# Kernel optimization log

Hardware: AMD Instinct MI355X
Metric: run time of the kernel (lower is better)

Reference implementation:

```python
import jax, jax.numpy as jnp
import numpy as np

N = 50000      # n_nodes == ninput
E = 800000     # edges
NHID = 96
N_INTER = 6
EPS = 1e-12


def _l2norm(x):
    # F.normalize(x, p=2, dim=1) with eps=1e-12
    n = jnp.linalg.norm(x, axis=1, keepdims=True)
    return x / jnp.maximum(n, EPS)


def _sage(x, src, dst, Wl, bl, Wr, n):
    # PyG SAGEConv (mean aggr): lin_l(mean_{j in N(i)} x_j) + lin_r(x_i)
    agg = jax.ops.segment_sum(x[src], dst, num_segments=n)          # [N, nhid]
    deg = jax.ops.segment_sum(jnp.ones((src.shape[0],), x.dtype), dst, num_segments=n)
    agg = agg / jnp.maximum(deg, 1.0)[:, None]
    return agg @ Wl + bl + x @ Wr


def _mlp(x, W1, b1, W2, b2, W3, b3):
    # GNN-Bet score MLP (eval mode, dropout p=0): nhid -> 2*nhid -> 2*nhid -> 1
    h = jax.nn.relu(x @ W1 + b1)
    h = jax.nn.relu(h @ W2 + b2)
    return h @ W3 + b3


def setup_inputs() -> dict:
    key = jax.random.key(0)
    ks = jax.random.split(key, 16)
    s = 0.05
    inp = {
        'edge_index1': jax.random.randint(ks[0], (2, E), 0, N, dtype=jnp.int32),
        'edge_vals1': jax.random.uniform(ks[1], (E,), dtype=jnp.float32),
        'edge_index2': jax.random.randint(ks[2], (2, E), 0, N, dtype=jnp.int32),
        # GNN_Layer_Init: weight [ninput=N, nhid], bias [nhid]
        'gc1_W': jax.random.normal(ks[3], (N, NHID), dtype=jnp.float32) * s,
        'gc1_b': jnp.zeros((NHID,), jnp.float32),
        # 7 SAGEConv layers (6 intermediate + gc_last), stacked
        'sage_Wl': jax.random.normal(ks[4], (7, NHID, NHID), dtype=jnp.float32) * s,
        'sage_bl': jnp.zeros((7, NHID), jnp.float32),
        'sage_Wr': jax.random.normal(ks[5], (7, NHID, NHID), dtype=jnp.float32) * s,
        # score MLP
        'mlp_W1': jax.random.normal(ks[6], (NHID, 2 * NHID), dtype=jnp.float32) * s,
        'mlp_b1': jnp.zeros((2 * NHID,), jnp.float32),
        'mlp_W2': jax.random.normal(ks[7], (2 * NHID, 2 * NHID), dtype=jnp.float32) * s,
        'mlp_b2': jnp.zeros((2 * NHID,), jnp.float32),
        'mlp_W3': jax.random.normal(ks[8], (2 * NHID, 1), dtype=jnp.float32) * s,
        'mlp_b3': jnp.zeros((1,), jnp.float32),
    }
    return inp


def reference(edge_index1, edge_vals1, edge_index2, gc1_W, gc1_b,
              sage_Wl, sage_bl, sage_Wr,
              mlp_W1, mlp_b1, mlp_W2, mlp_b2, mlp_W3, mlp_b3):
    # gc1: spmm(adj1, W) -> out[i] = sum_j adj1[i,j] * W[j]
    dst1, src1 = edge_index1[0], edge_index1[1]
    h0 = jax.ops.segment_sum(gc1_W[src1] * edge_vals1[:, None], dst1, num_segments=N) + gc1_b
    x2_1 = _l2norm(jax.nn.relu(h0))

    src2, dst2 = edge_index2[0], edge_index2[1]

    # main trunk: 6 intermediate SAGE layers applied sequentially
    x = x2_1
    for i in range(N_INTER):
        x = _l2norm(jax.nn.relu(_sage(x, src2, dst2, sage_Wl[i], sage_bl[i], sage_Wr[i], N)))
    x_last = jax.nn.relu(_sage(x, src2, dst2, sage_Wl[N_INTER], sage_bl[N_INTER], sage_Wr[N_INTER], N))

    # scores: MLP on x2_1, on each intermediate layer applied once to x2_1, and on x_last
    score = _mlp(x2_1, mlp_W1, mlp_b1, mlp_W2, mlp_b2, mlp_W3, mlp_b3)
    for i in range(N_INTER):
        xi = _l2norm(jax.nn.relu(_sage(x2_1, src2, dst2, sage_Wl[i], sage_bl[i], sage_Wr[i], N)))
        score = score + _mlp(xi, mlp_W1, mlp_b1, mlp_W2, mlp_b2, mlp_W3, mlp_b3)
    score = score + _mlp(x_last, mlp_W1, mlp_b1, mlp_W2, mlp_b2, mlp_W3, mlp_b3)
    return score  # [N, 1]
```

## Files before the change

### kernel.cpp

```cpp
#include <hip/hip_runtime.h>

#define NH 96
#define NH2 192

typedef __attribute__((ext_vector_type(8))) short short8;
typedef __attribute__((ext_vector_type(4))) float f32x4;

__device__ __forceinline__ unsigned short f2b(float f) {
  unsigned u = __float_as_uint(f);
  unsigned r = (u + 0x7FFFu + ((u >> 16) & 1u)) >> 16;
  return (unsigned short)r;
}
__device__ __forceinline__ float blo(unsigned w) { return __uint_as_float(w << 16); }
__device__ __forceinline__ float bhi(unsigned w) { return __uint_as_float(w & 0xFFFF0000u); }
__device__ __forceinline__ float b2f(short v) { return __uint_as_float(((unsigned)(unsigned short)v) << 16); }

__device__ __forceinline__ unsigned cvt_pk(float lo, float hi) {
  unsigned r;
  asm("v_cvt_pk_bf16_f32 %0, %1, %2" : "=v"(r) : "v"(lo), "v"(hi));
  return r;
}

__device__ __forceinline__ short8 u4_to_s8(int a, int b, int c, int d) {
  union { int u[4]; short8 s; } x;
  x.u[0] = a; x.u[1] = b; x.u[2] = c; x.u[3] = d;
  return x.s;
}

#define MFMA(a, b, c) __builtin_amdgcn_mfma_f32_16x16x32_bf16((a), (b), (c), 0, 0, 0)
#define WFRAG(p, idx) (*(const short8*)((p) + ((idx) << 9) + (l << 3)))

__device__ __forceinline__ void stage(unsigned short* dst, const unsigned short* src, int nshorts, int tid) {
  const uint4* s = (const uint4*)src;
  uint4* d = (uint4*)dst;
  int nv = nshorts >> 3;
  for (int i = tid; i < nv; i += 256) d[i] = s[i];
}

__device__ __forceinline__ short8 xchg(unsigned p0lo, unsigned p0hi, unsigned p1lo, unsigned p1hi,
                                       int srcA, int srcB, int hi) {
  int a0 = __shfl((int)p0lo, srcA), a1 = __shfl((int)p0hi, srcA);
  int c0 = __shfl((int)p1lo, srcA), c1 = __shfl((int)p1hi, srcA);
  int b0 = __shfl((int)p0lo, srcB), b1 = __shfl((int)p0hi, srcB);
  int d0 = __shfl((int)p1lo, srcB), d1 = __shfl((int)p1hi, srcB);
  return u4_to_s8(hi ? c0 : a0, hi ? c1 : a1, hi ? d0 : b0, hi ? d1 : b1);
}


__global__ void k_count(const int* __restrict__ dst1, const int* __restrict__ dst2,
                        int* __restrict__ cnt1, int* __restrict__ cnt2, int E) {
  int e = blockIdx.x * blockDim.x + threadIdx.x;
  if (e < E) {
    atomicAdd(&cnt1[dst1[e]], 1);
    atomicAdd(&cnt2[dst2[e]], 1);
  }
}


__global__ __launch_bounds__(256) void k_scanA(const int* __restrict__ cnt1, const int* __restrict__ cnt2,
                                               int* __restrict__ bs, int n) {
  int seg = blockIdx.y;
  const int* cnt = seg ? cnt2 : cnt1;
  int t = threadIdx.x;
  int idx = blockIdx.x * 1024 + t * 4;
  int sum = 0;
  if (idx + 3 < n) {
    int4 v = *(const int4*)(cnt + idx);
    sum = v.x + v.y + v.z + v.w;
  } else {
    for (int j = 0; j < 4; ++j) if (idx + j < n) sum += cnt[idx + j];
  }
  __shared__ int s[256];
  s[t] = sum;
  __syncthreads();
  for (int off = 128; off > 0; off >>= 1) {
    if (t < off) s[t] += s[t + off];
    __syncthreads();
  }
  if (t == 0) bs[seg * 64 + blockIdx.x] = s[0];
}

__global__ __launch_bounds__(128) void k_scanB(int* __restrict__ bs, int* __restrict__ rp1,
                                               int* __restrict__ rp2, int nb, int n) {
  int w = threadIdx.x >> 6, l = threadIdx.x & 63;
  int v = (l < nb) ? bs[w * 64 + l] : 0;
  int incl = v;
  for (int off = 1; off < 64; off <<= 1) {
    int u = __shfl_up(incl, off);
    if (l >= off) incl += u;
  }
  if (l < nb) bs[w * 64 + l] = incl - v;
  if (l == 63) {
    int* rp = w ? rp2 : rp1;
    rp[n] = incl;
  }
}

__global__ __launch_bounds__(256) void k_scanC(const int* __restrict__ cnt1, const int* __restrict__ cnt2,
                                               const int* __restrict__ bs,
                                               int* __restrict__ rp1, int* __restrict__ cur1,
                                               int* __restrict__ rp2, int* __restrict__ cur2, int n) {
  int seg = blockIdx.y;
  const int* cnt = seg ? cnt2 : cnt1;
  int* rp = seg ? rp2 : rp1;
  int* cur = seg ? cur2 : cur1;
  int t = threadIdx.x;
  int idx = blockIdx.x * 1024 + t * 4;
  int v[4] = {0, 0, 0, 0};
  if (idx + 3 < n) {
    int4 q = *(const int4*)(cnt + idx);
    v[0] = q.x; v[1] = q.y; v[2] = q.z; v[3] = q.w;
  } else {
    for (int j = 0; j < 4; ++j) if (idx + j < n) v[j] = cnt[idx + j];
  }
  int tsum = v[0] + v[1] + v[2] + v[3];
  __shared__ int s[256];
  s[t] = tsum;
  __syncthreads();
  for (int off = 1; off < 256; off <<= 1) {
    int u = (t >= off) ? s[t - off] : 0;
    __syncthreads();
    s[t] += u;
    __syncthreads();
  }
  int run = (t == 0 ? 0 : s[t - 1]) + bs[seg * 64 + blockIdx.x];
  for (int j = 0; j < 4; ++j) {
    if (idx + j < n) {
      rp[idx + j] = run;
      cur[idx + j] = run;
      run += v[j];
    }
  }
}

__global__ __launch_bounds__(1024) void k_scan(const int* __restrict__ cnt, int* __restrict__ rp,
                                               int* __restrict__ cur, int n) {
  __shared__ int s[1024];
  int tid = threadIdx.x;
  int chunk = (n + 1023) >> 10;
  int beg = tid * chunk;
  int end = min(beg + chunk, n);
  int sum = 0;
  for (int i = beg; i < end; ++i) sum += cnt[i];
  s[tid] = sum;
  __syncthreads();
  for (int off = 1; off < 1024; off <<= 1) {
    int v = (tid >= off) ? s[tid - off] : 0;
    __syncthreads();
    s[tid] += v;
    __syncthreads();
  }
  int excl = (tid == 0) ? 0 : s[tid - 1];
  for (int i = beg; i < end; ++i) { rp[i] = excl; cur[i] = excl; excl += cnt[i]; }
  if (tid == 1023) rp[n] = s[1023];
}

__global__ void k_scatter(const int* __restrict__ d1, const int* __restrict__ s1, const float* __restrict__ v1,
                          int* __restrict__ cur1, int2* __restrict__ c1sv,
                          const int* __restrict__ s2, const int* __restrict__ d2,
                          int* __restrict__ cur2, int* __restrict__ c2s, int E, int psize) {
  int p = blockIdx.x & 7;
  int e = (blockIdx.x >> 3) * blockDim.x + threadIdx.x;
  if (e >= E) return;
  int lo = p * psize, hi = lo + psize;
  int d = d1[e];
  if (d >= lo && d < hi) {
    int pos = atomicAdd(&cur1[d], 1);
    c1sv[pos] = make_int2(s1[e], __float_as_int(v1[e]));
  }
  int dd = d2[e];
  if (dd >= lo && dd < hi) {
    int pos = atomicAdd(&cur2[dd], 1);
    c2s[pos] = s2[e];
  }
}


__global__ void k_cvtgw(const float* __restrict__ W, unsigned short* __restrict__ Wb, int total) {
  int i = (blockIdx.x * blockDim.x + threadIdx.x) * 4;
  if (i + 3 < total) {
    float4 v = *(const float4*)(W + i);
    ushort4 o;
    o.x = f2b(v.x); o.y = f2b(v.y); o.z = f2b(v.z); o.w = f2b(v.w);
    *(ushort4*)(Wb + i) = o;
  }
}

__global__ void k_packw(const float* __restrict__ Wl, const float* __restrict__ Wr,
                        const float* __restrict__ W1, const float* __restrict__ W2,
                        unsigned short* __restrict__ Wlp, unsigned short* __restrict__ Wrp,
                        unsigned short* __restrict__ W1p, unsigned short* __restrict__ W2p) {
  int t = blockIdx.x * blockDim.x + threadIdx.x;
  if (t < 129024) {
    bool isR = t >= 64512;
    int u = isR ? t - 64512 : t;
    int i = u / 9216, v = u % 9216;
    int tt = v / 1536, r = v % 1536;
    int kf = r / 512, w = r % 512, l = w >> 3, j = w & 7;
    int c = l & 15, g = l >> 4;
    int k = kf * 32 + g * 8 + j, nn = tt * 16 + c;
    float val = (isR ? Wr : Wl)[i * 9216 + k * 96 + nn];
    (isR ? Wrp : Wlp)[u] = f2b(val);
  } else if (t < 147456) {
    int u = t - 129024;
    int tt = u / 1536, r = u % 1536;
    int kf = r / 512, w = r % 512, l = w >> 3, j = w & 7;
    int c = l & 15, g = l >> 4;
    int k = kf * 32 + g * 8 + j, nn = tt * 16 + c;
    W1p[u] = f2b(W1[k * 192 + nn]);
  } else if (t < 184320) {
    int u = t - 147456;
    int tt = u / 3072, r = u % 3072;
    int kf = r / 512, w = r % 512, l = w >> 3, j = w & 7;
    int c = l & 15, g = l >> 4;
    int k = kf * 32 + g * 8 + j, nn = tt * 16 + c;
    W2p[u] = f2b(W2[k * 192 + nn]);
  }
}


__global__ __launch_bounds__(256) void k_gc1(const int* __restrict__ rp, const int2* __restrict__ cv,
                                             const unsigned short* __restrict__ Wb,
                                             const float* __restrict__ b, unsigned short* __restrict__ out, int n) {
  int gw = (blockIdx.x * 256 + threadIdx.x) >> 6;
  int l = threadIdx.x & 63;
  if (gw >= n) return;
  int s = rp[gw], e = rp[gw + 1];
  bool act = l < 48;
  float a0 = 0.f, a1 = 0.f, b0 = 0.f, b1 = 0.f, c0 = 0.f, c1 = 0.f, d0 = 0.f, d1 = 0.f;
  int i = s;
  for (; i + 3 < e; i += 4) {
    int2 q0 = cv[i], q1 = cv[i + 1], q2 = cv[i + 2], q3 = cv[i + 3];
    if (act) {
      unsigned w0 = *(const unsigned*)(Wb + (size_t)q0.x * NH + 2 * l);
      unsigned w1 = *(const unsigned*)(Wb + (size_t)q1.x * NH + 2 * l);
      unsigned w2 = *(const unsigned*)(Wb + (size_t)q2.x * NH + 2 * l);
      unsigned w3 = *(const unsigned*)(Wb + (size_t)q3.x * NH + 2 * l);
      float v0 = __int_as_float(q0.y), v1 = __int_as_float(q1.y);
      float v2 = __int_as_float(q2.y), v3 = __int_as_float(q3.y);
      a0 = fmaf(v0, blo(w0), a0); a1 = fmaf(v0, bhi(w0), a1);
      b0 = fmaf(v1, blo(w1), b0); b1 = fmaf(v1, bhi(w1), b1);
      c0 = fmaf(v2, blo(w2), c0); c1 = fmaf(v2, bhi(w2), c1);
      d0 = fmaf(v3, blo(w3), d0); d1 = fmaf(v3, bhi(w3), d1);
    }
  }
  for (; i < e; ++i) {
    int2 q0 = cv[i];
    if (act) {
      unsigned w0 = *(const unsigned*)(Wb + (size_t)q0.x * NH + 2 * l);
      float v0 = __int_as_float(q0.y);
      a0 = fmaf(v0, blo(w0), a0); a1 = fmaf(v0, bhi(w0), a1);
    }
  }
  a0 += b0 + c0 + d0; a1 += b1 + c1 + d1;
  if (act) {
    a0 = fmaxf(a0 + b[2 * l], 0.f);
    a1 = fmaxf(a1 + b[2 * l + 1], 0.f);
  } else { a0 = a1 = 0.f; }
  float ss = a0 * a0 + a1 * a1;
#pragma unroll
  for (int o = 1; o < 64; o <<= 1) ss += __shfl_xor(ss, o);
  float sc = 1.f / fmaxf(sqrtf(ss), 1e-12f);
  if (act) {
    unsigned pk = ((unsigned)f2b(a1 * sc) << 16) | f2b(a0 * sc);
    ((unsigned*)out)[(size_t)gw * 48 + l] = pk;
  }
}


__global__ __launch_bounds__(256) void k_agg(const int* __restrict__ rp, const int* __restrict__ csrc,
                                             const unsigned short* __restrict__ X,
                                             unsigned short* __restrict__ out, int n) {
  int gw = (blockIdx.x * 256 + threadIdx.x) >> 6;
  int l = threadIdx.x & 63;
  if (gw >= n) return;
  int s = rp[gw], e = rp[gw + 1];
  bool act = l < 48;
  float a0 = 0.f, a1 = 0.f, b0 = 0.f, b1 = 0.f, c0 = 0.f, c1 = 0.f, d0 = 0.f, d1 = 0.f;
  int i = s;
  for (; i + 3 < e; i += 4) {
    int s0 = csrc[i], s1 = csrc[i + 1], s2 = csrc[i + 2], s3 = csrc[i + 3];
    if (act) {
      unsigned w0 = *(const unsigned*)(X + (size_t)s0 * NH + 2 * l);
      unsigned w1 = *(const unsigned*)(X + (size_t)s1 * NH + 2 * l);
      unsigned w2 = *(const unsigned*)(X + (size_t)s2 * NH + 2 * l);
      unsigned w3 = *(const unsigned*)(X + (size_t)s3 * NH + 2 * l);
      a0 += blo(w0); a1 += bhi(w0);
      b0 += blo(w1); b1 += bhi(w1);
      c0 += blo(w2); c1 += bhi(w2);
      d0 += blo(w3); d1 += bhi(w3);
    }
  }
  for (; i < e; ++i) {
    int s0 = csrc[i];
    if (act) {
      unsigned w0 = *(const unsigned*)(X + (size_t)s0 * NH + 2 * l);
      a0 += blo(w0); a1 += bhi(w0);
    }
  }
  a0 += b0 + c0 + d0; a1 += b1 + c1 + d1;
  float inv = 1.f / fmaxf((float)(e - s), 1.f);
  if (act) {
    unsigned pk = ((unsigned)f2b(a1 * inv) << 16) | f2b(a0 * inv);
    ((unsigned*)out)[(size_t)gw * 48 + l] = pk;
  }
}


template <int EPI>
__global__ __launch_bounds__(256) void k_sageagg(const int* __restrict__ rp, const int* __restrict__ csrc,
                                                 const unsigned short* __restrict__ X,
                                                 const unsigned short* __restrict__ Wlp,
                                                 const unsigned short* __restrict__ Wrp,
                                                 const float* __restrict__ bias,
                                                 unsigned short* __restrict__ Y, int n) {
  __shared__ __align__(16) unsigned short sw[18432];
  int tid = threadIdx.x;
  int l = tid & 63;
  int m0 = (blockIdx.x * 4 + (tid >> 6)) * 16;
  int c = l & 15, g = l >> 4;

  stage(sw, Wlp, 9216, tid);
  stage(sw + 9216, Wrp, 9216, tid);
  __syncthreads();

  int nd = min(m0 + c, n - 1);
  int s = rp[nd], e = rp[nd + 1];

  float aa[3][8], bb[3][8];
#pragma unroll
  for (int kf = 0; kf < 3; ++kf)
#pragma unroll
    for (int j = 0; j < 8; ++j) { aa[kf][j] = 0.f; bb[kf][j] = 0.f; }

  const unsigned short* Xg = X + g * 8;
  int i = s;
  for (; i + 1 < e; i += 2) {
    const unsigned short* xr0 = Xg + (size_t)csrc[i] * NH;
    const unsigned short* xr1 = Xg + (size_t)csrc[i + 1] * NH;
    short8 a0 = *(const short8*)(xr0);
    short8 a1 = *(const short8*)(xr0 + 32);
    short8 a2 = *(const short8*)(xr0 + 64);
    short8 b0 = *(const short8*)(xr1);
    short8 b1 = *(const short8*)(xr1 + 32);
    short8 b2 = *(const short8*)(xr1 + 64);
#pragma unroll
    for (int j = 0; j < 8; ++j) {
      aa[0][j] += b2f(a0[j]); aa[1][j] += b2f(a1[j]); aa[2][j] += b2f(a2[j]);
      bb[0][j] += b2f(b0[j]); bb[1][j] += b2f(b1[j]); bb[2][j] += b2f(b2[j]);
    }
  }
  if (i < e) {
    const unsigned short* xr0 = Xg + (size_t)csrc[i] * NH;
    short8 a0 = *(const short8*)(xr0);
    short8 a1 = *(const short8*)(xr0 + 32);
    short8 a2 = *(const short8*)(xr0 + 64);
#pragma unroll
    for (int j = 0; j < 8; ++j) {
      aa[0][j] += b2f(a0[j]); aa[1][j] += b2f(a1[j]); aa[2][j] += b2f(a2[j]);
    }
  }
  float inv = 1.f / fmaxf((float)(e - s), 1.f);
  short8 af[3];
#pragma unroll
  for (int kf = 0; kf < 3; ++kf)
#pragma unroll
    for (int j = 0; j < 8; ++j) af[kf][j] = (short)f2b((aa[kf][j] + bb[kf][j]) * inv);

  size_t aoff = (size_t)nd * NH + g * 8;
  short8 xf[3];
#pragma unroll
  for (int kf = 0; kf < 3; ++kf) xf[kf] = *(const short8*)(X + aoff + kf * 32);

  f32x4 acc[6];
#pragma unroll
  for (int t = 0; t < 6; ++t) acc[t] = (f32x4){0.f, 0.f, 0.f, 0.f};
#pragma unroll
  for (int kf = 0; kf < 3; ++kf) {
#pragma unroll
    for (int t = 0; t < 6; ++t) {
      short8 wlf = WFRAG(sw, t * 3 + kf);
      acc[t] = MFMA(wlf, af[kf], acc[t]);
    }
#pragma unroll
    for (int t = 0; t < 6; ++t) {
      short8 wrf = WFRAG(sw + 9216, t * 3 + kf);
      acc[t] = MFMA(wrf, xf[kf], acc[t]);
    }
  }

  float v[6][4];
  float ss = 0.f;
#pragma unroll
  for (int t = 0; t < 6; ++t) {
    float4 bv = *(const float4*)(bias + t * 16 + g * 4);
#pragma unroll
    for (int r = 0; r < 4; ++r) {
      float x = fmaxf(acc[t][r] + ((const float*)&bv)[r], 0.f);
      v[t][r] = x;
      ss = fmaf(x, x, ss);
    }
  }
  if (EPI == 0) {
    ss += __shfl_xor(ss, 16);
    ss += __shfl_xor(ss, 32);
    float sc = 1.f / fmaxf(sqrtf(ss), 1e-12f);
#pragma unroll
    for (int t = 0; t < 6; ++t)
#pragma unroll
      for (int r = 0; r < 4; ++r) v[t][r] *= sc;
  }
  if (m0 + c < n) {
    unsigned short* yr = Y + (size_t)(m0 + c) * NH;
#pragma unroll
    for (int t = 0; t < 6; ++t)
      *(uint2*)(yr + t * 16 + g * 4) = make_uint2(cvt_pk(v[t][0], v[t][1]), cvt_pk(v[t][2], v[t][3]));
  }
}


__global__ __launch_bounds__(256) void k_mlp(const unsigned short* __restrict__ X,
                                             const unsigned short* __restrict__ W1p, const float* __restrict__ b1,
                                             const unsigned short* __restrict__ W2p, const float* __restrict__ b2,
                                             const float* __restrict__ W3, const float* __restrict__ b3,
                                             float* __restrict__ score, int n) {
  __shared__ __align__(16) unsigned short sw[18432];
  int tid = threadIdx.x;
  int l = tid & 63;
  int m0 = (blockIdx.x * 4 + (tid >> 6)) * 32;
  int c = l & 15, g = l >> 4;
  int srcA = c + ((g & 1) << 5), srcB = srcA + 16, hi = g >> 1;
  int rA = min(m0 + c, n - 1), rB = min(m0 + 16 + c, n - 1);

  stage(sw, W1p, 18432, tid);

  short8 xf[2][3];
#pragma unroll
  for (int kf = 0; kf < 3; ++kf) {
    xf[0][kf] = *(const short8*)(X + (size_t)rA * NH + kf * 32 + g * 8);
    xf[1][kf] = *(const short8*)(X + (size_t)rB * NH + kf * 32 + g * 8);
  }
  __syncthreads();

  unsigned pk1[2][12][2];
#pragma unroll
  for (int t = 0; t < 12; ++t) {
    f32x4 a0 = (f32x4){0.f, 0.f, 0.f, 0.f};
    f32x4 a1 = (f32x4){0.f, 0.f, 0.f, 0.f};
#pragma unroll
    for (int kf = 0; kf < 3; ++kf) {
      short8 wf = WFRAG(sw, t * 3 + kf);
      a0 = MFMA(wf, xf[0][kf], a0);
      a1 = MFMA(wf, xf[1][kf], a1);
    }
    float4 bv = *(const float4*)(b1 + t * 16 + g * 4);
    pk1[0][t][0] = cvt_pk(fmaxf(a0[0] + bv.x, 0.f), fmaxf(a0[1] + bv.y, 0.f));
    pk1[0][t][1] = cvt_pk(fmaxf(a0[2] + bv.z, 0.f), fmaxf(a0[3] + bv.w, 0.f));
    pk1[1][t][0] = cvt_pk(fmaxf(a1[0] + bv.x, 0.f), fmaxf(a1[1] + bv.y, 0.f));
    pk1[1][t][1] = cvt_pk(fmaxf(a1[2] + bv.z, 0.f), fmaxf(a1[3] + bv.w, 0.f));
  }

  short8 af2[2][6];
#pragma unroll
  for (int kf = 0; kf < 6; ++kf) {
    af2[0][kf] = xchg(pk1[0][2 * kf][0], pk1[0][2 * kf][1], pk1[0][2 * kf + 1][0], pk1[0][2 * kf + 1][1], srcA, srcB, hi);
    af2[1][kf] = xchg(pk1[1][2 * kf][0], pk1[1][2 * kf][1], pk1[1][2 * kf + 1][0], pk1[1][2 * kf + 1][1], srcA, srcB, hi);
  }

  float sv0 = 0.f, sv1 = 0.f;
#pragma unroll
  for (int h = 0; h < 2; ++h) {
    __syncthreads();
    stage(sw, W2p + h * 18432, 18432, tid);
    __syncthreads();
#pragma unroll
    for (int tt = 0; tt < 6; ++tt) {
      int t = h * 6 + tt;
      f32x4 a0 = (f32x4){0.f, 0.f, 0.f, 0.f};
      f32x4 a1 = (f32x4){0.f, 0.f, 0.f, 0.f};
#pragma unroll
      for (int kf = 0; kf < 6; ++kf) {
        short8 wf = WFRAG(sw, tt * 6 + kf);
        a0 = MFMA(wf, af2[0][kf], a0);
        a1 = MFMA(wf, af2[1][kf], a1);
      }
      float4 bv = *(const float4*)(b2 + t * 16 + g * 4);
      float4 wv3 = *(const float4*)(W3 + t * 16 + g * 4);
#pragma unroll
      for (int r = 0; r < 4; ++r) {
        sv0 = fmaf(fmaxf(a0[r] + ((const float*)&bv)[r], 0.f), ((const float*)&wv3)[r], sv0);
        sv1 = fmaf(fmaxf(a1[r] + ((const float*)&bv)[r], 0.f), ((const float*)&wv3)[r], sv1);
      }
    }
  }
  sv0 += __shfl_xor(sv0, 16); sv0 += __shfl_xor(sv0, 32);
  sv1 += __shfl_xor(sv1, 16); sv1 += __shfl_xor(sv1, 32);
  if (g == 0) {
    float b3v = b3[0];
    if (m0 + c < n) score[m0 + c] += sv0 + b3v;
    if (m0 + 16 + c < n) score[m0 + 16 + c] += sv1 + b3v;
  }
}


__global__ __launch_bounds__(256) void k_branch(const unsigned short* __restrict__ Ag,
                                                const unsigned short* __restrict__ X21,
                                                const unsigned short* __restrict__ Wlp,
                                                const unsigned short* __restrict__ Wrp,
                                                const float* __restrict__ sbl,
                                                const unsigned short* __restrict__ W1p, const float* __restrict__ b1,
                                                const unsigned short* __restrict__ W2p, const float* __restrict__ b2,
                                                const float* __restrict__ W3, const float* __restrict__ b3,
                                                unsigned short* __restrict__ Xb, float* __restrict__ score,
                                                int n, int gblk) {
  __shared__ __align__(16) unsigned short sw[18432];
  int bb = blockIdx.x / gblk;
  int blk = blockIdx.x - bb * gblk;
  int tid = threadIdx.x;
  int l = tid & 63;
  int m0 = (blk * 4 + (tid >> 6)) * 32;
  int c = l & 15, g = l >> 4;
  int srcA = c + ((g & 1) << 5), srcB = srcA + 16, hi = g >> 1;
  int rA = min(m0 + c, n - 1), rB = min(m0 + 16 + c, n - 1);
  size_t aoffA = (size_t)rA * NH + g * 8, aoffB = (size_t)rB * NH + g * 8;

  const float* bl = sbl + (size_t)bb * NH;

  stage(sw, Wlp + (size_t)bb * 9216, 9216, tid);
  stage(sw + 9216, Wrp + (size_t)bb * 9216, 9216, tid);

  short8 agf[2][3], xf[2][3];
#pragma unroll
  for (int kf = 0; kf < 3; ++kf) {
    agf[0][kf] = *(const short8*)(Ag + aoffA + kf * 32);
    agf[1][kf] = *(const short8*)(Ag + aoffB + kf * 32);
    xf[0][kf] = *(const short8*)(X21 + aoffA + kf * 32);
    xf[1][kf] = *(const short8*)(X21 + aoffB + kf * 32);
  }
  __syncthreads();

  float v[2][6][4];
  float ss0 = 0.f, ss1 = 0.f;
#pragma unroll
  for (int t = 0; t < 6; ++t) {
    f32x4 a0 = (f32x4){0.f, 0.f, 0.f, 0.f};
    f32x4 a1 = (f32x4){0.f, 0.f, 0.f, 0.f};
#pragma unroll
    for (int kf = 0; kf < 3; ++kf) {
      short8 wlf = WFRAG(sw, t * 3 + kf);
      a0 = MFMA(wlf, agf[0][kf], a0);
      a1 = MFMA(wlf, agf[1][kf], a1);
      short8 wrf = WFRAG(sw + 9216, t * 3 + kf);
      a0 = MFMA(wrf, xf[0][kf], a0);
      a1 = MFMA(wrf, xf[1][kf], a1);
    }
    float4 bv = *(const float4*)(bl + t * 16 + g * 4);
#pragma unroll
    for (int r = 0; r < 4; ++r) {
      float x0 = fmaxf(a0[r] + ((const float*)&bv)[r], 0.f);
      float x1 = fmaxf(a1[r] + ((const float*)&bv)[r], 0.f);
      v[0][t][r] = x0; ss0 = fmaf(x0, x0, ss0);
      v[1][t][r] = x1; ss1 = fmaf(x1, x1, ss1);
    }
  }
  ss0 += __shfl_xor(ss0, 16); ss0 += __shfl_xor(ss0, 32);
  ss1 += __shfl_xor(ss1, 16); ss1 += __shfl_xor(ss1, 32);
  float sc0 = 1.f / fmaxf(sqrtf(ss0), 1e-12f);
  float sc1 = 1.f / fmaxf(sqrtf(ss1), 1e-12f);

  unsigned pk[2][6][2];
#pragma unroll
  for (int t = 0; t < 6; ++t) {
    pk[0][t][0] = cvt_pk(v[0][t][0] * sc0, v[0][t][1] * sc0);
    pk[0][t][1] = cvt_pk(v[0][t][2] * sc0, v[0][t][3] * sc0);
    pk[1][t][0] = cvt_pk(v[1][t][0] * sc1, v[1][t][1] * sc1);
    pk[1][t][1] = cvt_pk(v[1][t][2] * sc1, v[1][t][3] * sc1);
  }
  if (bb == 0) {
    if (m0 + c < n) {
      unsigned short* yr = Xb + (size_t)(m0 + c) * NH;
#pragma unroll
      for (int t = 0; t < 6; ++t) *(uint2*)(yr + t * 16 + g * 4) = make_uint2(pk[0][t][0], pk[0][t][1]);
    }
    if (m0 + 16 + c < n) {
      unsigned short* yr = Xb + (size_t)(m0 + 16 + c) * NH;
#pragma unroll
      for (int t = 0; t < 6; ++t) *(uint2*)(yr + t * 16 + g * 4) = make_uint2(pk[1][t][0], pk[1][t][1]);
    }
  }

  __syncthreads();
  stage(sw, W1p, 18432, tid);
  short8 af1[2][3];
#pragma unroll
  for (int kf = 0; kf < 3; ++kf) {
    af1[0][kf] = xchg(pk[0][2 * kf][0], pk[0][2 * kf][1], pk[0][2 * kf + 1][0], pk[0][2 * kf + 1][1], srcA, srcB, hi);
    af1[1][kf] = xchg(pk[1][2 * kf][0], pk[1][2 * kf][1], pk[1][2 * kf + 1][0], pk[1][2 * kf + 1][1], srcA, srcB, hi);
  }
  __syncthreads();
  unsigned pk1[2][12][2];
#pragma unroll
  for (int t = 0; t < 12; ++t) {
    f32x4 a0 = (f32x4){0.f, 0.f, 0.f, 0.f};
    f32x4 a1 = (f32x4){0.f, 0.f, 0.f, 0.f};
#pragma unroll
    for (int kf = 0; kf < 3; ++kf) {
      short8 wf = WFRAG(sw, t * 3 + kf);
      a0 = MFMA(wf, af1[0][kf], a0);
      a1 = MFMA(wf, af1[1][kf], a1);
    }
    float4 bv = *(const float4*)(b1 + t * 16 + g * 4);
    pk1[0][t][0] = cvt_pk(fmaxf(a0[0] + bv.x, 0.f), fmaxf(a0[1] + bv.y, 0.f));
    pk1[0][t][1] = cvt_pk(fmaxf(a0[2] + bv.z, 0.f), fmaxf(a0[3] + bv.w, 0.f));
    pk1[1][t][0] = cvt_pk(fmaxf(a1[0] + bv.x, 0.f), fmaxf(a1[1] + bv.y, 0.f));
    pk1[1][t][1] = cvt_pk(fmaxf(a1[2] + bv.z, 0.f), fmaxf(a1[3] + bv.w, 0.f));
  }

  short8 af2[2][6];
#pragma unroll
  for (int kf = 0; kf < 6; ++kf) {
    af2[0][kf] = xchg(pk1[0][2 * kf][0], pk1[0][2 * kf][1], pk1[0][2 * kf + 1][0], pk1[0][2 * kf + 1][1], srcA, srcB, hi);
    af2[1][kf] = xchg(pk1[1][2 * kf][0], pk1[1][2 * kf][1], pk1[1][2 * kf + 1][0], pk1[1][2 * kf + 1][1], srcA, srcB, hi);
  }
  float sv0 = 0.f, sv1 = 0.f;
#pragma unroll
  for (int h = 0; h < 2; ++h) {
    __syncthreads();
    stage(sw, W2p + h * 18432, 18432, tid);
    __syncthreads();
#pragma unroll
    for (int tt = 0; tt < 6; ++tt) {
      int t = h * 6 + tt;
      f32x4 a0 = (f32x4){0.f, 0.f, 0.f, 0.f};
      f32x4 a1 = (f32x4){0.f, 0.f, 0.f, 0.f};
#pragma unroll
      for (int kf = 0; kf < 6; ++kf) {
        short8 wf = WFRAG(sw, tt * 6 + kf);
        a0 = MFMA(wf, af2[0][kf], a0);
        a1 = MFMA(wf, af2[1][kf], a1);
      }
      float4 bv = *(const float4*)(b2 + t * 16 + g * 4);
      float4 wv3 = *(const float4*)(W3 + t * 16 + g * 4);
#pragma unroll
      for (int r = 0; r < 4; ++r) {
        sv0 = fmaf(fmaxf(a0[r] + ((const float*)&bv)[r], 0.f), ((const float*)&wv3)[r], sv0);
        sv1 = fmaf(fmaxf(a1[r] + ((const float*)&bv)[r], 0.f), ((const float*)&wv3)[r], sv1);
      }
    }
  }
  sv0 += __shfl_xor(sv0, 16); sv0 += __shfl_xor(sv0, 32);
  sv1 += __shfl_xor(sv1, 16); sv1 += __shfl_xor(sv1, 32);
  if (g == 0) {
    float b3v = b3[0];
    if (m0 + c < n) atomicAdd(&score[m0 + c], sv0 + b3v);
    if (m0 + 16 + c < n) atomicAdd(&score[m0 + 16 + c], sv1 + b3v);
  }
}


extern "C" void kernel_launch(void* const* d_in, const int* in_sizes, int n_in,
                              void* d_out, int out_size, void* d_ws, size_t ws_size,
                              hipStream_t stream) {
  const int* ei1 = (const int*)d_in[0];
  const float* ev1 = (const float*)d_in[1];
  const int* ei2 = (const int*)d_in[2];
  const float* gW = (const float*)d_in[3];
  const float* gb = (const float*)d_in[4];
  const float* sWl = (const float*)d_in[5];
  const float* sbl = (const float*)d_in[6];
  const float* sWr = (const float*)d_in[7];
  const float* W1 = (const float*)d_in[8];
  const float* b1 = (const float*)d_in[9];
  const float* W2 = (const float*)d_in[10];
  const float* b2 = (const float*)d_in[11];
  const float* W3 = (const float*)d_in[12];
  const float* b3 = (const float*)d_in[13];
  float* score = (float*)d_out;

  const int E = in_sizes[0] / 2;
  const int n = in_sizes[3] / NH;

  const int* d1 = ei1;
  const int* s1 = ei1 + E;
  const int* s2 = ei2;
  const int* d2 = ei2 + E;

  char* w = (char*)d_ws;
  auto alloc = [&](size_t bytes) {
    char* p = w;
    w += (bytes + 255) & ~(size_t)255;
    return p;
  };
  int* cnt1 = (int*)alloc((size_t)n * 4);
  int* cnt2 = (int*)alloc((size_t)n * 4);
  int* cur1 = (int*)alloc((size_t)n * 4);
  int* cur2 = (int*)alloc((size_t)n * 4);
  int* rp1 = (int*)alloc((size_t)(n + 1) * 4);
  int* rp2 = (int*)alloc((size_t)(n + 1) * 4);
  int* bs = (int*)alloc(128 * 4);
  int2* c1sv = (int2*)alloc((size_t)E * 8);
  int* c2s = (int*)alloc((size_t)E * 4);
  unsigned short* gwb = (unsigned short*)alloc((size_t)n * NH * 2);
  unsigned short* wlp = (unsigned short*)alloc((size_t)7 * NH * NH * 2);
  unsigned short* wrp = (unsigned short*)alloc((size_t)7 * NH * NH * 2);
  unsigned short* w1p = (unsigned short*)alloc((size_t)NH * NH2 * 2);
  unsigned short* w2p = (unsigned short*)alloc((size_t)NH2 * NH2 * 2);
  unsigned short* x21 = (unsigned short*)alloc((size_t)n * NH * 2);
  unsigned short* Ag = (unsigned short*)alloc((size_t)n * NH * 2);
  unsigned short* xb = (unsigned short*)alloc((size_t)n * NH * 2);
  unsigned short* tb = (unsigned short*)alloc((size_t)n * NH * 2);

  size_t zbytes = (size_t)((char*)cur1 - (char*)cnt1) + (size_t)n * 4;
  hipMemsetAsync(cnt1, 0, zbytes, stream);
  hipMemsetAsync(score, 0, (size_t)n * 4, stream);

  int eb = (E + 255) / 256;
  int nb4 = (n + 3) / 4;
  int sblk = (n + 63) / 64;
  int gblk = (n + 127) / 128;
  int psize = (n + 7) / 8;
  int nb1024 = (n + 1023) / 1024;

  k_count<<<eb, 256, 0, stream>>>(d1, d2, cnt1, cnt2, E);
  if (nb1024 <= 64) {
    k_scanA<<<dim3(nb1024, 2), 256, 0, stream>>>(cnt1, cnt2, bs, n);
    k_scanB<<<1, 128, 0, stream>>>(bs, rp1, rp2, nb1024, n);
    k_scanC<<<dim3(nb1024, 2), 256, 0, stream>>>(cnt1, cnt2, bs, rp1, cur1, rp2, cur2, n);
  } else {
    k_scan<<<1, 1024, 0, stream>>>(cnt1, rp1, cur1, n);
    k_scan<<<1, 1024, 0, stream>>>(cnt2, rp2, cur2, n);
  }
  k_scatter<<<eb * 8, 256, 0, stream>>>(d1, s1, ev1, cur1, c1sv, s2, d2, cur2, c2s, E, psize);

  k_cvtgw<<<(n * NH / 4 + 255) / 256, 256, 0, stream>>>(gW, gwb, n * NH);
  k_packw<<<720, 256, 0, stream>>>(sWl, sWr, W1, W2, wlp, wrp, w1p, w2p);

  k_gc1<<<nb4, 256, 0, stream>>>(rp1, c1sv, gwb, gb, x21, n);

  k_mlp<<<gblk, 256, 0, stream>>>(x21, w1p, b1, w2p, b2, W3, b3, score, n);

  k_agg<<<nb4, 256, 0, stream>>>(rp2, c2s, x21, Ag, n);

  k_branch<<<6 * gblk, 256, 0, stream>>>(Ag, x21, wlp, wrp, sbl, w1p, b1, w2p, b2, W3, b3,
                                         xb, score, n, gblk);

  unsigned short* xc = xb;
  unsigned short* xn = tb;
  for (int i = 1; i < 6; ++i) {
    k_sageagg<0><<<sblk, 256, 0, stream>>>(rp2, c2s, xc, wlp + (size_t)i * 9216,
                                           wrp + (size_t)i * 9216, sbl + (size_t)i * NH, xn, n);
    unsigned short* tmp = xc; xc = xn; xn = tmp;
  }

  k_sageagg<1><<<sblk, 256, 0, stream>>>(rp2, c2s, xc, wlp + (size_t)6 * 9216,
                                         wrp + (size_t)6 * 9216, sbl + (size_t)6 * NH, xn, n);
  k_mlp<<<gblk, 256, 0, stream>>>(xn, w1p, b1, w2p, b2, W3, b3, score, n);

  (void)n_in; (void)out_size; (void)ws_size;
}
```

Baseline: 559.8 us.

## Fold x2_1 MLP into branch kernel, merge prep kernels, partition count atomics

Partitions the degree-count atomics into 8 destination ranges, the same scheme the scatter kernel uses, to improve atomic locality. Merges the gc1 weight bf16 conversion and the weight packing into one prep kernel. Drops the separate MLP launch on x2_1 by adding a seventh branch group to k_branch that feeds x2_1 directly into the MLP. k_branch now uses 512-thread blocks covering 256 rows each. The changes save launches and share weight staging across more rows, at the cost of fewer blocks and a larger block size that may lower occupancy.

```diff
diff --git a/kernel.cpp b/kernel.cpp
--- a/kernel.cpp
+++ b/kernel.cpp
@@ -30,11 +30,12 @@
 #define MFMA(a, b, c) __builtin_amdgcn_mfma_f32_16x16x32_bf16((a), (b), (c), 0, 0, 0)
 #define WFRAG(p, idx) (*(const short8*)((p) + ((idx) << 9) + (l << 3)))
 
-__device__ __forceinline__ void stage(unsigned short* dst, const unsigned short* src, int nshorts, int tid) {
+__device__ __forceinline__ void stage(unsigned short* dst, const unsigned short* src, int nshorts,
+                                      int tid, int nt) {
   const uint4* s = (const uint4*)src;
   uint4* d = (uint4*)dst;
   int nv = nshorts >> 3;
-  for (int i = tid; i < nv; i += 256) d[i] = s[i];
+  for (int i = tid; i < nv; i += nt) d[i] = s[i];
 }
 
 __device__ __forceinline__ short8 xchg(unsigned p0lo, unsigned p0hi, unsigned p1lo, unsigned p1hi,
@@ -48,12 +49,15 @@
 
 
 __global__ void k_count(const int* __restrict__ dst1, const int* __restrict__ dst2,
-                        int* __restrict__ cnt1, int* __restrict__ cnt2, int E) {
-  int e = blockIdx.x * blockDim.x + threadIdx.x;
-  if (e < E) {
-    atomicAdd(&cnt1[dst1[e]], 1);
-    atomicAdd(&cnt2[dst2[e]], 1);
-  }
+                        int* __restrict__ cnt1, int* __restrict__ cnt2, int E, int psize) {
+  int p = blockIdx.x & 7;
+  int e = (blockIdx.x >> 3) * blockDim.x + threadIdx.x;
+  if (e >= E) return;
+  int lo = p * psize, hi = lo + psize;
+  int d = dst1[e];
+  if (d >= lo && d < hi) atomicAdd(&cnt1[d], 1);
+  int dd = dst2[e];
+  if (dd >= lo && dd < hi) atomicAdd(&cnt2[dd], 1);
 }
 
 
@@ -176,20 +180,12 @@
 }
 
 
-__global__ void k_cvtgw(const float* __restrict__ W, unsigned short* __restrict__ Wb, int total) {
-  int i = (blockIdx.x * blockDim.x + threadIdx.x) * 4;
-  if (i + 3 < total) {
-    float4 v = *(const float4*)(W + i);
-    ushort4 o;
-    o.x = f2b(v.x); o.y = f2b(v.y); o.z = f2b(v.z); o.w = f2b(v.w);
-    *(ushort4*)(Wb + i) = o;
-  }
-}
-
-__global__ void k_packw(const float* __restrict__ Wl, const float* __restrict__ Wr,
-                        const float* __restrict__ W1, const float* __restrict__ W2,
-                        unsigned short* __restrict__ Wlp, unsigned short* __restrict__ Wrp,
-                        unsigned short* __restrict__ W1p, unsigned short* __restrict__ W2p) {
+__global__ void k_prep(const float* __restrict__ Wl, const float* __restrict__ Wr,
+                       const float* __restrict__ W1, const float* __restrict__ W2,
+                       const float* __restrict__ gW,
+                       unsigned short* __restrict__ Wlp, unsigned short* __restrict__ Wrp,
+                       unsigned short* __restrict__ W1p, unsigned short* __restrict__ W2p,
+                       unsigned short* __restrict__ gwb, int gtotal) {
   int t = blockIdx.x * blockDim.x + threadIdx.x;
   if (t < 129024) {
     bool isR = t >= 64512;
@@ -215,6 +211,14 @@
     int c = l & 15, g = l >> 4;
     int k = kf * 32 + g * 8 + j, nn = tt * 16 + c;
     W2p[u] = f2b(W2[k * 192 + nn]);
+  } else {
+    int i = (t - 184320) * 4;
+    if (i + 3 < gtotal) {
+      float4 v = *(const float4*)(gW + i);
+      ushort4 o;
+      o.x = f2b(v.x); o.y = f2b(v.y); o.z = f2b(v.z); o.w = f2b(v.w);
+      *(ushort4*)(gwb + i) = o;
+    }
   }
 }
 
@@ -320,8 +324,8 @@
   int m0 = (blockIdx.x * 4 + (tid >> 6)) * 16;
   int c = l & 15, g = l >> 4;
 
-  stage(sw, Wlp, 9216, tid);
-  stage(sw + 9216, Wrp, 9216, tid);
+  stage(sw, Wlp, 9216, tid, 256);
+  stage(sw + 9216, Wrp, 9216, tid, 256);
   __syncthreads();
 
   int nd = min(m0 + c, n - 1);
@@ -432,7 +436,7 @@
   int srcA = c + ((g & 1) << 5), srcB = srcA + 16, hi = g >> 1;
   int rA = min(m0 + c, n - 1), rB = min(m0 + 16 + c, n - 1);
 
-  stage(sw, W1p, 18432, tid);
+  stage(sw, W1p, 18432, tid, 256);
 
   short8 xf[2][3];
 #pragma unroll
@@ -471,7 +475,7 @@
 #pragma unroll
   for (int h = 0; h < 2; ++h) {
     __syncthreads();
-    stage(sw, W2p + h * 18432, 18432, tid);
+    stage(sw, W2p + h * 18432, 18432, tid, 256);
     __syncthreads();
 #pragma unroll
     for (int tt = 0; tt < 6; ++tt) {
@@ -503,7 +507,7 @@
 }
 
 
-__global__ __launch_bounds__(256) void k_branch(const unsigned short* __restrict__ Ag,
+__global__ __launch_bounds__(512) void k_branch(const unsigned short* __restrict__ Ag,
                                                 const unsigned short* __restrict__ X21,
                                                 const unsigned short* __restrict__ Wlp,
                                                 const unsigned short* __restrict__ Wrp,
@@ -512,92 +516,103 @@
                                                 const unsigned short* __restrict__ W2p, const float* __restrict__ b2,
                                                 const float* __restrict__ W3, const float* __restrict__ b3,
                                                 unsigned short* __restrict__ Xb, float* __restrict__ score,
-                                                int n, int gblk) {
+                                                int n, int nblk) {
   __shared__ __align__(16) unsigned short sw[18432];
-  int bb = blockIdx.x / gblk;
-  int blk = blockIdx.x - bb * gblk;
+  int bb = blockIdx.x / nblk;
+  int blk = blockIdx.x - bb * nblk;
   int tid = threadIdx.x;
   int l = tid & 63;
-  int m0 = (blk * 4 + (tid >> 6)) * 32;
+  int m0 = (blk * 8 + (tid >> 6)) * 32;
   int c = l & 15, g = l >> 4;
   int srcA = c + ((g & 1) << 5), srcB = srcA + 16, hi = g >> 1;
   int rA = min(m0 + c, n - 1), rB = min(m0 + 16 + c, n - 1);
   size_t aoffA = (size_t)rA * NH + g * 8, aoffB = (size_t)rB * NH + g * 8;
 
-  const float* bl = sbl + (size_t)bb * NH;
-
-  stage(sw, Wlp + (size_t)bb * 9216, 9216, tid);
-  stage(sw + 9216, Wrp + (size_t)bb * 9216, 9216, tid);
-
-  short8 agf[2][3], xf[2][3];
-#pragma unroll
-  for (int kf = 0; kf < 3; ++kf) {
-    agf[0][kf] = *(const short8*)(Ag + aoffA + kf * 32);
-    agf[1][kf] = *(const short8*)(Ag + aoffB + kf * 32);
-    xf[0][kf] = *(const short8*)(X21 + aoffA + kf * 32);
-    xf[1][kf] = *(const short8*)(X21 + aoffB + kf * 32);
-  }
-  __syncthreads();
-
-  float v[2][6][4];
-  float ss0 = 0.f, ss1 = 0.f;
-#pragma unroll
-  for (int t = 0; t < 6; ++t) {
-    f32x4 a0 = (f32x4){0.f, 0.f, 0.f, 0.f};
-    f32x4 a1 = (f32x4){0.f, 0.f, 0.f, 0.f};
+  short8 af1[2][3];
+
+  if (bb < 6) {
+    const float* bl = sbl + (size_t)bb * NH;
+    stage(sw, Wlp + (size_t)bb * 9216, 9216, tid, 512);
+    stage(sw + 9216, Wrp + (size_t)bb * 9216, 9216, tid, 512);
+
+    short8 agf[2][3], xf[2][3];
 #pragma unroll
     for (int kf = 0; kf < 3; ++kf) {
-      short8 wlf = WFRAG(sw, t * 3 + kf);
-      a0 = MFMA(wlf, agf[0][kf], a0);
-      a1 = MFMA(wlf, agf[1][kf], a1);
-      short8 wrf = WFRAG(sw + 9216, t * 3 + kf);
-      a0 = MFMA(wrf, xf[0][kf], a0);
-      a1 = MFMA(wrf, xf[1][kf], a1);
-    }
-    float4 bv = *(const float4*)(bl + t * 16 + g * 4);
-#pragma unroll
-    for (int r = 0; r < 4; ++r) {
-      float x0 = fmaxf(a0[r] + ((const float*)&bv)[r], 0.f);
-      float x1 = fmaxf(a1[r] + ((const float*)&bv)[r], 0.f);
-      v[0][t][r] = x0; ss0 = fmaf(x0, x0, ss0);
-      v[1][t][r] = x1; ss1 = fmaf(x1, x1, ss1);
-    }
-  }
-  ss0 += __shfl_xor(ss0, 16); ss0 += __shfl_xor(ss0, 32);
-  ss1 += __shfl_xor(ss1, 16); ss1 += __shfl_xor(ss1, 32);
-  float sc0 = 1.f / fmaxf(sqrtf(ss0), 1e-12f);
-  float sc1 = 1.f / fmaxf(sqrtf(ss1), 1e-12f);
-
-  unsigned pk[2][6][2];
-#pragma unroll
-  for (int t = 0; t < 6; ++t) {
-    pk[0][t][0] = cvt_pk(v[0][t][0] * sc0, v[0][t][1] * sc0);
-    pk[0][t][1] = cvt_pk(v[0][t][2] * sc0, v[0][t][3] * sc0);
-    pk[1][t][0] = cvt_pk(v[1][t][0] * sc1, v[1][t][1] * sc1);
-    pk[1][t][1] = cvt_pk(v[1][t][2] * sc1, v[1][t][3] * sc1);
-  }
-  if (bb == 0) {
-    if (m0 + c < n) {
-      unsigned short* yr = Xb + (size_t)(m0 + c) * NH;
-#pragma unroll
-      for (int t = 0; t < 6; ++t) *(uint2*)(yr + t * 16 + g * 4) = make_uint2(pk[0][t][0], pk[0][t][1]);
-    }
-    if (m0 + 16 + c < n) {
-      unsigned short* yr = Xb + (size_t)(m0 + 16 + c) * NH;
-#pragma unroll
-      for (int t = 0; t < 6; ++t) *(uint2*)(yr + t * 16 + g * 4) = make_uint2(pk[1][t][0], pk[1][t][1]);
-    }
-  }
-
-  __syncthreads();
-  stage(sw, W1p, 18432, tid);
-  short8 af1[2][3];
-#pragma unroll
-  for (int kf = 0; kf < 3; ++kf) {
-    af1[0][kf] = xchg(pk[0][2 * kf][0], pk[0][2 * kf][1], pk[0][2 * kf + 1][0], pk[0][2 * kf + 1][1], srcA, srcB, hi);
-    af1[1][kf] = xchg(pk[1][2 * kf][0], pk[1][2 * kf][1], pk[1][2 * kf + 1][0], pk[1][2 * kf + 1][1], srcA, srcB, hi);
-  }
-  __syncthreads();
+      agf[0][kf] = *(const short8*)(Ag + aoffA + kf * 32);
+      agf[1][kf] = *(const short8*)(Ag + aoffB + kf * 32);
+      xf[0][kf] = *(const short8*)(X21 + aoffA + kf * 32);
+      xf[1][kf] = *(const short8*)(X21 + aoffB + kf * 32);
+    }
+    __syncthreads();
+
+    float v[2][6][4];
+    float ss0 = 0.f, ss1 = 0.f;
+#pragma unroll
+    for (int t = 0; t < 6; ++t) {
+      f32x4 a0 = (f32x4){0.f, 0.f, 0.f, 0.f};
+      f32x4 a1 = (f32x4){0.f, 0.f, 0.f, 0.f};
+#pragma unroll
+      for (int kf = 0; kf < 3; ++kf) {
+        short8 wlf = WFRAG(sw, t * 3 + kf);
+        a0 = MFMA(wlf, agf[0][kf], a0);
+        a1 = MFMA(wlf, agf[1][kf], a1);
+        short8 wrf = WFRAG(sw + 9216, t * 3 + kf);
+        a0 = MFMA(wrf, xf[0][kf], a0);
+        a1 = MFMA(wrf, xf[1][kf], a1);
+      }
+      float4 bv = *(const float4*)(bl + t * 16 + g * 4);
+#pragma unroll
+      for (int r = 0; r < 4; ++r) {
+        float x0 = fmaxf(a0[r] + ((const float*)&bv)[r], 0.f);
+        float x1 = fmaxf(a1[r] + ((const float*)&bv)[r], 0.f);
+        v[0][t][r] = x0; ss0 = fmaf(x0, x0, ss0);
+        v[1][t][r] = x1; ss1 = fmaf(x1, x1, ss1);
+      }
+    }
+    ss0 += __shfl_xor(ss0, 16); ss0 += __shfl_xor(ss0, 32);
+    ss1 += __shfl_xor(ss1, 16); ss1 += __shfl_xor(ss1, 32);
+    float sc0 = 1.f / fmaxf(sqrtf(ss0), 1e-12f);
+    float sc1 = 1.f / fmaxf(sqrtf(ss1), 1e-12f);
+
+    unsigned pk[2][6][2];
+#pragma unroll
+    for (int t = 0; t < 6; ++t) {
+      pk[0][t][0] = cvt_pk(v[0][t][0] * sc0, v[0][t][1] * sc0);
+      pk[0][t][1] = cvt_pk(v[0][t][2] * sc0, v[0][t][3] * sc0);
+      pk[1][t][0] = cvt_pk(v[1][t][0] * sc1, v[1][t][1] * sc1);
+      pk[1][t][1] = cvt_pk(v[1][t][2] * sc1, v[1][t][3] * sc1);
+    }
+    if (bb == 0) {
+      if (m0 + c < n) {
+        unsigned short* yr = Xb + (size_t)(m0 + c) * NH;
+#pragma unroll
+        for (int t = 0; t < 6; ++t) *(uint2*)(yr + t * 16 + g * 4) = make_uint2(pk[0][t][0], pk[0][t][1]);
+      }
+      if (m0 + 16 + c < n) {
+        unsigned short* yr = Xb + (size_t)(m0 + 16 + c) * NH;
+#pragma unroll
+        for (int t = 0; t < 6; ++t) *(uint2*)(yr + t * 16 + g * 4) = make_uint2(pk[1][t][0], pk[1][t][1]);
+      }
+    }
+
+    __syncthreads();
+    stage(sw, W1p, 18432, tid, 512);
+#pragma unroll
+    for (int kf = 0; kf < 3; ++kf) {
+      af1[0][kf] = xchg(pk[0][2 * kf][0], pk[0][2 * kf][1], pk[0][2 * kf + 1][0], pk[0][2 * kf + 1][1], srcA, srcB, hi);
+      af1[1][kf] = xchg(pk[1][2 * kf][0], pk[1][2 * kf][1], pk[1][2 * kf + 1][0], pk[1][2 * kf + 1][1], srcA, srcB, hi);
+    }
+    __syncthreads();
+  } else {
+#pragma unroll
+    for (int kf = 0; kf < 3; ++kf) {
+      af1[0][kf] = *(const short8*)(X21 + aoffA + kf * 32);
+      af1[1][kf] = *(const short8*)(X21 + aoffB + kf * 32);
+    }
+    stage(sw, W1p, 18432, tid, 512);
+    __syncthreads();
+  }
+
   unsigned pk1[2][12][2];
 #pragma unroll
   for (int t = 0; t < 12; ++t) {
@@ -626,7 +641,7 @@
 #pragma unroll
   for (int h = 0; h < 2; ++h) {
     __syncthreads();
-    stage(sw, W2p + h * 18432, 18432, tid);
+    stage(sw, W2p + h * 18432, 18432, tid, 512);
     __syncthreads();
 #pragma unroll
     for (int tt = 0; tt < 6; ++tt) {
@@ -718,10 +733,13 @@
   int nb4 = (n + 3) / 4;
   int sblk = (n + 63) / 64;
   int gblk = (n + 127) / 128;
+  int nblk = (n + 255) / 256;
   int psize = (n + 7) / 8;
   int nb1024 = (n + 1023) / 1024;
-
-  k_count<<<eb, 256, 0, stream>>>(d1, d2, cnt1, cnt2, E);
+  int gtotal = n * NH;
+  int prep_threads = 184320 + gtotal / 4;
+
+  k_count<<<eb * 8, 256, 0, stream>>>(d1, d2, cnt1, cnt2, E, psize);
   if (nb1024 <= 64) {
     k_scanA<<<dim3(nb1024, 2), 256, 0, stream>>>(cnt1, cnt2, bs, n);
     k_scanB<<<1, 128, 0, stream>>>(bs, rp1, rp2, nb1024, n);
@@ -732,17 +750,15 @@
   }
   k_scatter<<<eb * 8, 256, 0, stream>>>(d1, s1, ev1, cur1, c1sv, s2, d2, cur2, c2s, E, psize);
 
-  k_cvtgw<<<(n * NH / 4 + 255) / 256, 256, 0, stream>>>(gW, gwb, n * NH);
-  k_packw<<<720, 256, 0, stream>>>(sWl, sWr, W1, W2, wlp, wrp, w1p, w2p);
+  k_prep<<<(prep_threads + 255) / 256, 256, 0, stream>>>(sWl, sWr, W1, W2, gW,
+                                                         wlp, wrp, w1p, w2p, gwb, gtotal);
 
   k_gc1<<<nb4, 256, 0, stream>>>(rp1, c1sv, gwb, gb, x21, n);
 
-  k_mlp<<<gblk, 256, 0, stream>>>(x21, w1p, b1, w2p, b2, W3, b3, score, n);
-
   k_agg<<<nb4, 256, 0, stream>>>(rp2, c2s, x21, Ag, n);
 
-  k_branch<<<6 * gblk, 256, 0, stream>>>(Ag, x21, wlp, wrp, sbl, w1p, b1, w2p, b2, W3, b3,
-                                         xb, score, n, gblk);
+  k_branch<<<7 * nblk, 512, 0, stream>>>(Ag, x21, wlp, wrp, sbl, w1p, b1, w2p, b2, W3, b3,
+                                         xb, score, n, nblk);
 
   unsigned short* xc = xb;
   unsigned short* xn = tb;
```

Result: no change. 553.4 us (-1.1%).
